# Kernel tuning notes

Hardware: AMD Instinct MI355X
Metric: run time of the kernel (lower is better)

The kernel has to match this reference:

```python
import jax, jax.numpy as jnp
import numpy as np
from collections import defaultdict

H = 24; W = 24          # patch grid
B0 = 64                 # original batch (len(batch_id))
B = 128                 # total batch incl. augmented copies
C_IN = 256; HID = 128; HEADS_S = 2; OUT = 256; K = 9; NCLS = 8


def _build_space_edges():
    # knn_graph on the normalized meshgrid coords; identical for every image -> offset copies.
    P = H * W
    coords = np.stack(np.meshgrid(np.arange(H), np.arange(W), indexing='ij'), -1).reshape(-1, 2).astype(np.float32)
    cn = coords / coords.max()
    d = ((cn[:, None, :] - cn[None, :, :]) ** 2).sum(-1)
    np.fill_diagonal(d, np.inf)              # loop=False
    nbr = np.argsort(d, axis=1)[:, :K]       # [P, K] neighbor (source) ids
    off = (np.arange(B0) * P)[:, None, None]
    src = (nbr[None] + off).reshape(-1)
    dst = (np.broadcast_to(np.arange(P)[:, None], (P, K))[None] + off).reshape(-1)
    return np.stack([src, dst]).astype(np.int64)


def _build_view_edges(bid_all):
    groups = defaultdict(list)
    for i, c in enumerate(bid_all.tolist()):
        groups[c].append(i)
    ei = []
    for c, mem in groups.items():
        for a in range(len(mem)):
            for b in range(a + 1, len(mem)):
                i, j = mem[a], mem[b]
                if i >= B0 and j >= B0:
                    continue               # skip augmented-augmented pairs
                ei.append((i, j)); ei.append((j, i))
    return np.array(ei, dtype=np.int64).T


def setup_inputs() -> dict:
    key = jax.random.key(0)
    ks = jax.random.split(key, 8)
    bid = np.repeat(np.arange(NCLS), B0 // NCLS).astype(np.int64)
    bid_all = np.concatenate([bid, bid])
    s = 0.05
    return {
        'x': jax.random.normal(ks[0], (B, C_IN, H, W), jnp.float32),
        'batch_id_all': jnp.asarray(bid_all),
        'batch_id': jnp.asarray(bid),
        'edge_index_space': jnp.asarray(_build_space_edges()),
        'edge_index_view': jnp.asarray(_build_view_edges(bid_all)),
        'W_space': jax.random.normal(ks[1], (C_IN, HEADS_S * HID), jnp.float32) * s,
        'att_src_space': jax.random.normal(ks[2], (HEADS_S, HID), jnp.float32) * s,
        'att_dst_space': jax.random.normal(ks[3], (HEADS_S, HID), jnp.float32) * s,
        'bias_space': jnp.zeros((HEADS_S * HID,), jnp.float32),
        'W_view': jax.random.normal(ks[4], (HEADS_S * HID, OUT), jnp.float32) * s,
        'att_src_view': jax.random.normal(ks[5], (1, OUT), jnp.float32) * s,
        'att_dst_view': jax.random.normal(ks[6], (1, OUT), jnp.float32) * s,
        'bias_view': jnp.zeros((OUT,), jnp.float32),
    }


def _gat(xn, edges, Wm, a_src, a_dst, bias, heads, outc):
    # PyG GATConv: linear -> per-edge leaky_relu attn -> segment softmax over dst -> scatter-add
    N = xn.shape[0]
    loops = jnp.arange(N, dtype=edges.dtype)              # add_self_loops=True
    src = jnp.concatenate([edges[0], loops])
    dst = jnp.concatenate([edges[1], loops])
    h = (xn @ Wm).reshape(N, heads, outc)                 # [N, H, C]
    a_s = jnp.sum(h * a_src[None], -1)                    # [N, H]
    a_d = jnp.sum(h * a_dst[None], -1)
    e = jax.nn.leaky_relu(a_s[src] + a_d[dst], 0.2)       # [E, H]
    m = jax.ops.segment_max(e, dst, num_segments=N)
    ee = jnp.exp(e - m[dst])
    ssum = jax.ops.segment_sum(ee, dst, num_segments=N)
    alpha = ee / (ssum[dst] + 1e-16)
    out = jax.ops.segment_sum(h[src] * alpha[..., None], dst, num_segments=N)
    return out.reshape(N, heads * outc) + bias            # concat=True


def reference(x, batch_id_all, batch_id, edge_index_space, edge_index_view,
              W_space, att_src_space, att_dst_space, bias_space,
              W_view, att_src_view, att_dst_view, bias_view):
    P = H * W
    node = x[:B0].transpose(0, 2, 3, 1).reshape(-1, C_IN)                # [B0*P, C_in]
    x_space = _gat(node, edge_index_space, W_space, att_src_space,
                   att_dst_space, bias_space, HEADS_S, HID)              # [B0*P, 256]
    emb = x_space.reshape(B0, P, -1).mean(axis=1)                        # per-image mean pool
    emb_all = emb[jnp.arange(B) % B0]                                    # augmented i -> i % B0
    feat = _gat(emb_all, edge_index_view, W_view, att_src_view,
                att_dst_view, bias_view, 1, OUT)                         # [B, 256]
    C = feat.shape[1]
    x_view = 0.5 * x_space.reshape(B0, P, C) + 0.5 * feat[:B0][:, None, :]
    # torch does .reshape(-1, C).view(B, C, H, W): a raw row-major reinterpret
    return x_view.reshape(B0, C, H, W)
```

## Files before the change

kernel.cpp:

```cpp
#include <hip/hip_runtime.h>

#define PGRID 576
#define NB0   64
#define CIN   256
#define KNN   9
#define NNODE (NB0 * PGRID)

typedef __attribute__((ext_vector_type(8))) short short8;
typedef __attribute__((ext_vector_type(4))) float f32x4;

__device__ __forceinline__ float bf2f(unsigned short u) {
    union { unsigned int i; float f; } v; v.i = ((unsigned int)u) << 16; return v.f;
}
__device__ __forceinline__ unsigned short f2b(float f) {
    unsigned int u = __float_as_uint(f);
    return (unsigned short)((u + 0x7FFFu + ((u >> 16) & 1u)) >> 16);
}

__global__ __launch_bounds__(256) void prep_w(const float* __restrict__ W,
                                              unsigned short* __restrict__ Wt) {
    __shared__ float tile[64][65];
    const int c0 = blockIdx.x * 64, j0 = blockIdx.y * 64;
    const int t = threadIdx.x, lo = t % 64, hi = t / 64;
#pragma unroll
    for (int r = 0; r < 16; ++r)
        tile[r * 4 + hi][lo] = W[(size_t)(c0 + r * 4 + hi) * 256 + j0 + lo];
    __syncthreads();
#pragma unroll
    for (int r = 0; r < 16; ++r)
        Wt[(size_t)(j0 + r * 4 + hi) * 256 + c0 + lo] = f2b(tile[lo][r * 4 + hi]);
}

__global__ __launch_bounds__(256) void gemm_fused(
    const float* __restrict__ x, const unsigned short* __restrict__ Wt,
    const float* __restrict__ att_src, const float* __restrict__ att_dst,
    unsigned short* __restrict__ h, float* __restrict__ as_, float* __restrict__ ad_) {
    __shared__ char ldsB[65536];
    const int bx = blockIdx.x;
    const int t  = threadIdx.x;
    const int b  = bx / 9;
    const int p0 = (bx % 9) * 64;
    const int n0 = bx * 64;
    const int l = t & 63, w = t >> 6;
    const int l4 = l >> 4, l15 = l & 15;
    const float* xb = x + (size_t)b * (CIN * PGRID);

    const int prow = p0 + w * 16 + l15;
    float a0[64];
#pragma unroll
    for (int ch = 0; ch < 2; ++ch)
#pragma unroll
        for (int q = 0; q < 4; ++q)
#pragma unroll
            for (int jj = 0; jj < 8; ++jj) {
                int c = ch * 128 + q * 32 + l4 * 8 + jj;
                a0[ch * 32 + q * 8 + jj] = xb[(size_t)c * PGRID + prow];
            }
    {
        const int jrow = t >> 4, g = t & 15;
#pragma unroll
        for (int i = 0; i < 16; ++i) {
            int j  = i * 16 + jrow;
            int gs = (g & 8) | ((g & 7) ^ (j & 7));
            __builtin_amdgcn_global_load_lds(
                (const char*)Wt + (size_t)j * 512 + gs * 16,
                ldsB + i * 4096 + (t & 192) * 16, 16, 0, 0);
        }
    }
    short8 apk[8];
#pragma unroll
    for (int cq = 0; cq < 8; ++cq) {
        short8 v;
#pragma unroll
        for (int jj = 0; jj < 8; ++jj) v[jj] = (short)f2b(a0[cq * 8 + jj]);
        apk[cq] = v;
    }
    f32x4 acc[16] = {};
    __syncthreads();
#pragma unroll
    for (int q = 0; q < 4; ++q) {
        const int gr = q * 4 + l4;
#pragma unroll
        for (int f = 0; f < 16; ++f) {
            int j  = f * 16 + l15;
            int gp = (gr & 8) | ((gr & 7) ^ (j & 7));
            short8 bf = *(const short8*)(ldsB + j * 256 + gp * 16);
            acc[f] = __builtin_amdgcn_mfma_f32_16x16x32_bf16(apk[q], bf, acc[f], 0, 0, 0);
        }
    }
    __syncthreads();
    {
        const int jrow = t >> 4, g = t & 15;
#pragma unroll
        for (int i = 0; i < 16; ++i) {
            int j  = i * 16 + jrow;
            int gs = (g & 8) | ((g & 7) ^ (j & 7));
            __builtin_amdgcn_global_load_lds(
                (const char*)Wt + (size_t)j * 512 + 256 + gs * 16,
                ldsB + i * 4096 + (t & 192) * 16, 16, 0, 0);
        }
    }
    __syncthreads();
#pragma unroll
    for (int q = 0; q < 4; ++q) {
        const int gr = q * 4 + l4;
#pragma unroll
        for (int f = 0; f < 16; ++f) {
            int j  = f * 16 + l15;
            int gp = (gr & 8) | ((gr & 7) ^ (j & 7));
            short8 bf = *(const short8*)(ldsB + j * 256 + gp * 16);
            acc[f] = __builtin_amdgcn_mfma_f32_16x16x32_bf16(apk[4 + q], bf, acc[f], 0, 0, 0);
        }
    }
    const int nb = n0 + w * 16 + l4 * 4;
#pragma unroll
    for (int f = 0; f < 16; ++f)
#pragma unroll
        for (int r = 0; r < 4; ++r)
            h[(size_t)(nb + r) * 256 + l15 + f * 16] = f2b(acc[f][r]);

    float av[16], dvv[16];
#pragma unroll
    for (int f = 0; f < 16; ++f) {
        av[f]  = att_src[f * 16 + l15];
        dvv[f] = att_dst[f * 16 + l15];
    }
#pragma unroll
    for (int r = 0; r < 4; ++r) {
        float s0 = 0.f, s1 = 0.f, d0 = 0.f, d1 = 0.f;
#pragma unroll
        for (int f = 0; f < 8; ++f)  { s0 += acc[f][r] * av[f];  d0 += acc[f][r] * dvv[f]; }
#pragma unroll
        for (int f = 8; f < 16; ++f) { s1 += acc[f][r] * av[f];  d1 += acc[f][r] * dvv[f]; }
#pragma unroll
        for (int m = 1; m < 16; m <<= 1) {
            s0 += __shfl_xor(s0, m); s1 += __shfl_xor(s1, m);
            d0 += __shfl_xor(d0, m); d1 += __shfl_xor(d1, m);
        }
        if (l15 == 0) {
            int n = nb + r;
            as_[n * 2] = s0; as_[n * 2 + 1] = s1;
            ad_[n * 2] = d0; ad_[n * 2 + 1] = d1;
        }
    }
}

__global__ __launch_bounds__(256) void space_gather(
    const unsigned short* __restrict__ h, const float* __restrict__ as_,
    const float* __restrict__ ad_, const int* __restrict__ esrc,
    const float* __restrict__ bias, unsigned short* __restrict__ xsb) {
    __shared__ int   s_src[2][10];
    __shared__ float s_e[2][10][2];
    const int t = threadIdx.x;
    const int node = t >> 7;
    const int idx  = t & 127;
    const int n = blockIdx.x * 2 + node;
    if (idx < 10) {
        int src = (idx < 9) ? esrc[(size_t)n * KNN + idx] : n;
        s_src[node][idx] = src;
        float e0 = as_[src * 2]     + ad_[n * 2];
        float e1 = as_[src * 2 + 1] + ad_[n * 2 + 1];
        s_e[node][idx][0] = e0 >= 0.f ? e0 : 0.2f * e0;
        s_e[node][idx][1] = e1 >= 0.f ? e1 : 0.2f * e1;
    }
    __syncthreads();
    const int j2 = idx * 2;
    const int head = idx >> 6;
    float m = -1e30f;
#pragma unroll
    for (int k = 0; k < 10; ++k) m = fmaxf(m, s_e[node][k][head]);
    float wgt[10]; float ssum = 0.f;
#pragma unroll
    for (int k = 0; k < 10; ++k) { wgt[k] = __expf(s_e[node][k][head] - m); ssum += wgt[k]; }
    const float inv = 1.f / (ssum + 1e-16f);
    float o0 = 0.f, o1 = 0.f;
#pragma unroll
    for (int k = 0; k < 10; ++k) {
        unsigned int v = *(const unsigned int*)(h + (size_t)s_src[node][k] * 256 + j2);
        o0 += wgt[k] * bf2f((unsigned short)(v & 0xffff));
        o1 += wgt[k] * bf2f((unsigned short)(v >> 16));
    }
    o0 = o0 * inv + bias[j2];
    o1 = o1 * inv + bias[j2 + 1];
    unsigned int pack = (unsigned int)f2b(o0) | ((unsigned int)f2b(o1) << 16);
    *(unsigned int*)(xsb + (size_t)n * 256 + j2) = pack;
}

__global__ __launch_bounds__(256) void pool_partial(const unsigned short* __restrict__ xsb,
                                                    float* __restrict__ embp) {
    __shared__ float red[2][256];
    const int b = blockIdx.x, seg = blockIdx.y;
    const int t = threadIdx.x;
    const int j2 = (t & 127) * 2, half = t >> 7;
    const unsigned short* base = xsb + ((size_t)b * PGRID + seg * 64 + half * 32) * 256 + j2;
    float s0 = 0.f, s1 = 0.f;
#pragma unroll 8
    for (int p = 0; p < 32; ++p) {
        unsigned int v = *(const unsigned int*)(base + (size_t)p * 256);
        s0 += bf2f((unsigned short)(v & 0xffff));
        s1 += bf2f((unsigned short)(v >> 16));
    }
    red[half][j2] = s0; red[half][j2 + 1] = s1;
    __syncthreads();
    if (half == 0) {
        float2 r;
        r.x = s0 + red[1][j2];
        r.y = s1 + red[1][j2 + 1];
        *(float2*)(embp + ((size_t)b * 9 + seg) * 256 + j2) = r;
    }
}

__global__ __launch_bounds__(256) void view_linear(const float* __restrict__ embp,
                                                   const float* __restrict__ Wv,
                                                   const float* __restrict__ att_s,
                                                   const float* __restrict__ att_d,
                                                   float* __restrict__ hv,
                                                   float* __restrict__ asv,
                                                   float* __restrict__ adv) {
    __shared__ float er[256];
    __shared__ float red[2][256];
    const int i = blockIdx.x;
    const int j = threadIdx.x;
    const int i64 = i & 63;
    float s = 0.f;
#pragma unroll
    for (int seg = 0; seg < 9; ++seg) s += embp[((size_t)i64 * 9 + seg) * 256 + j];
    er[j] = s * (1.f / 576.f);
    __syncthreads();
    float acc = 0.f;
    for (int c = 0; c < 256; ++c) acc += er[c] * Wv[c * 256 + j];
    hv[(size_t)i * 256 + j] = acc;
    red[0][j] = acc * att_s[j];
    red[1][j] = acc * att_d[j];
    __syncthreads();
    for (int off = 128; off > 0; off >>= 1) {
        if (j < off) { red[0][j] += red[0][j + off]; red[1][j] += red[1][j + off]; }
        __syncthreads();
    }
    if (j == 0) { asv[i] = red[0][0]; adv[i] = red[1][0]; }
}

__global__ __launch_bounds__(256) void view_gather(const float* __restrict__ hv,
                                                   const float* __restrict__ asv,
                                                   const float* __restrict__ adv,
                                                   const int* __restrict__ ev,
                                                   int Ev,
                                                   const float* __restrict__ bias,
                                                   float* __restrict__ feat) {
    __shared__ int cnt;
    __shared__ int s_src[32];
    const int d = blockIdx.x;
    const int t = threadIdx.x;
    if (t == 0) cnt = 0;
    __syncthreads();
    for (int e = t; e < Ev; e += 256) {
        if (ev[Ev + e] == d) {
            int pos = atomicAdd(&cnt, 1);
            s_src[pos] = ev[e];
        }
    }
    __syncthreads();
    const int ns = cnt;
    const float adval = adv[d];
    float m = -1e30f;
    float ev_[16];
#pragma unroll 1
    for (int k = 0; k < ns; ++k) {
        float e = asv[s_src[k]] + adval;
        e = e >= 0.f ? e : 0.2f * e;
        ev_[k] = e;
        m = fmaxf(m, e);
    }
    float eself = asv[d] + adval;
    eself = eself >= 0.f ? eself : 0.2f * eself;
    m = fmaxf(m, eself);
    float ssum = 0.f;
#pragma unroll 1
    for (int k = 0; k < ns; ++k) { ev_[k] = __expf(ev_[k] - m); ssum += ev_[k]; }
    float wself = __expf(eself - m);
    ssum += wself;
    const float inv = 1.f / (ssum + 1e-16f);
    float out = 0.f;
#pragma unroll 1
    for (int k = 0; k < ns; ++k) out += ev_[k] * hv[(size_t)s_src[k] * 256 + t];
    out += wself * hv[(size_t)d * 256 + t];
    feat[d * 256 + t] = out * inv + bias[t];
}

__global__ __launch_bounds__(256) void combine(const unsigned short* __restrict__ xsb,
                                               const float* __restrict__ feat,
                                               float* __restrict__ out, int ntot4) {
    int i = blockIdx.x * blockDim.x + threadIdx.x;
    if (i >= ntot4) return;
    size_t f = (size_t)i * 4;
    int b = (int)(f / (PGRID * 256));
    int j = (int)(f & 255);
    uint2 v = *(const uint2*)(xsb + f);
    float4 fb = *(const float4*)(feat + b * 256 + j);
    float4 o;
    o.x = 0.5f * (bf2f((unsigned short)(v.x & 0xffff)) + fb.x);
    o.y = 0.5f * (bf2f((unsigned short)(v.x >> 16))   + fb.y);
    o.z = 0.5f * (bf2f((unsigned short)(v.y & 0xffff)) + fb.z);
    o.w = 0.5f * (bf2f((unsigned short)(v.y >> 16))   + fb.w);
    *(float4*)(out + f) = o;
}

extern "C" void kernel_launch(void* const* d_in, const int* in_sizes, int n_in,
                              void* d_out, int out_size, void* d_ws, size_t ws_size,
                              hipStream_t stream) {
    const float* x        = (const float*)d_in[0];
    const int*   e_space  = (const int*)d_in[3];
    const int*   e_view   = (const int*)d_in[4];
    const float* W_space  = (const float*)d_in[5];
    const float* att_ss   = (const float*)d_in[6];
    const float* att_ds   = (const float*)d_in[7];
    const float* bias_s   = (const float*)d_in[8];
    const float* W_view   = (const float*)d_in[9];
    const float* att_sv   = (const float*)d_in[10];
    const float* att_dv   = (const float*)d_in[11];
    const float* bias_v   = (const float*)d_in[12];
    float* out = (float*)d_out;

    const int Ev = in_sizes[4] / 2;

    char* ws = (char*)d_ws;
    unsigned short* hbf = (unsigned short*)ws;
    unsigned short* Wt  = (unsigned short*)(ws + 18874368);
    unsigned short* xsb = (unsigned short*)(ws + 18874368 + 131072);
    float* as_  = (float*)(ws + 2 * 18874368 + 131072);
    float* ad_  = as_ + NNODE * 2;
    float* embp = ad_ + NNODE * 2;
    float* hv   = embp + 64 * 9 * 256;
    float* asv  = hv  + 128 * 256;
    float* adv  = asv + 128;
    float* feat = adv + 128;

    prep_w<<<dim3(4, 4), 256, 0, stream>>>(W_space, Wt);
    gemm_fused<<<576, 256, 0, stream>>>(x, Wt, att_ss, att_ds, hbf, as_, ad_);
    space_gather<<<NNODE / 2, 256, 0, stream>>>(hbf, as_, ad_, e_space, bias_s, xsb);
    pool_partial<<<dim3(NB0, 9), 256, 0, stream>>>(xsb, embp);
    view_linear<<<128, 256, 0, stream>>>(embp, W_view, att_sv, att_dv, hv, asv, adv);
    view_gather<<<NB0, 256, 0, stream>>>(hv, asv, adv, e_view, Ev, bias_v, feat);

    const int ntot4 = NB0 * PGRID * 256 / 4;
    combine<<<(ntot4 + 255) / 256, 256, 0, stream>>>(xsb, feat, out, ntot4);
}
```

Baseline: 209.9 us.

## Drop LDS staging in GEMM, widen gather and pool vector loads

The GEMM kernel no longer stages the bf16 weight in LDS. It swaps the MFMA operands so each lane loads weight fragments straight from global/L2 and writes h rows as packed 8-byte stores. The attention-score reduction now needs fewer shuffles. The space gather drops shared memory and syncthreads, handling one node per wavefront with 4 nodes per block and 8-byte loads, and pool_partial uses 4-element vector loads. This cuts LDS traffic, barriers and store transactions, but every block re-reads the weight from cache.

```diff
diff --git a/kernel.cpp b/kernel.cpp
--- a/kernel.cpp
+++ b/kernel.cpp
@@ -35,7 +35,6 @@
     const float* __restrict__ x, const unsigned short* __restrict__ Wt,
     const float* __restrict__ att_src, const float* __restrict__ att_dst,
     unsigned short* __restrict__ h, float* __restrict__ as_, float* __restrict__ ad_) {
-    __shared__ char ldsB[65536];
     const int bx = blockIdx.x;
     const int t  = threadIdx.x;
     const int b  = bx / 9;
@@ -44,29 +43,16 @@
     const int l = t & 63, w = t >> 6;
     const int l4 = l >> 4, l15 = l & 15;
     const float* xb = x + (size_t)b * (CIN * PGRID);
-
     const int prow = p0 + w * 16 + l15;
+
     float a0[64];
 #pragma unroll
-    for (int ch = 0; ch < 2; ++ch)
-#pragma unroll
-        for (int q = 0; q < 4; ++q)
-#pragma unroll
-            for (int jj = 0; jj < 8; ++jj) {
-                int c = ch * 128 + q * 32 + l4 * 8 + jj;
-                a0[ch * 32 + q * 8 + jj] = xb[(size_t)c * PGRID + prow];
-            }
-    {
-        const int jrow = t >> 4, g = t & 15;
-#pragma unroll
-        for (int i = 0; i < 16; ++i) {
-            int j  = i * 16 + jrow;
-            int gs = (g & 8) | ((g & 7) ^ (j & 7));
-            __builtin_amdgcn_global_load_lds(
-                (const char*)Wt + (size_t)j * 512 + gs * 16,
-                ldsB + i * 4096 + (t & 192) * 16, 16, 0, 0);
+    for (int cq = 0; cq < 8; ++cq)
+#pragma unroll
+        for (int jj = 0; jj < 8; ++jj) {
+            int c = cq * 32 + l4 * 8 + jj;
+            a0[cq * 8 + jj] = xb[(size_t)c * PGRID + prow];
         }
-    }
     short8 apk[8];
 #pragma unroll
     for (int cq = 0; cq < 8; ++cq) {
@@ -75,73 +61,46 @@
         for (int jj = 0; jj < 8; ++jj) v[jj] = (short)f2b(a0[cq * 8 + jj]);
         apk[cq] = v;
     }
+
     f32x4 acc[16] = {};
-    __syncthreads();
-#pragma unroll
-    for (int q = 0; q < 4; ++q) {
-        const int gr = q * 4 + l4;
+    const unsigned short* wbase = Wt + (size_t)l15 * 256 + l4 * 8;
+#pragma unroll
+    for (int q = 0; q < 8; ++q) {
 #pragma unroll
         for (int f = 0; f < 16; ++f) {
-            int j  = f * 16 + l15;
-            int gp = (gr & 8) | ((gr & 7) ^ (j & 7));
-            short8 bf = *(const short8*)(ldsB + j * 256 + gp * 16);
-            acc[f] = __builtin_amdgcn_mfma_f32_16x16x32_bf16(apk[q], bf, acc[f], 0, 0, 0);
+            short8 wf = *(const short8*)(wbase + (size_t)f * 4096 + q * 32);
+            acc[f] = __builtin_amdgcn_mfma_f32_16x16x32_bf16(wf, apk[q], acc[f], 0, 0, 0);
         }
     }
-    __syncthreads();
-    {
-        const int jrow = t >> 4, g = t & 15;
-#pragma unroll
-        for (int i = 0; i < 16; ++i) {
-            int j  = i * 16 + jrow;
-            int gs = (g & 8) | ((g & 7) ^ (j & 7));
-            __builtin_amdgcn_global_load_lds(
-                (const char*)Wt + (size_t)j * 512 + 256 + gs * 16,
-                ldsB + i * 4096 + (t & 192) * 16, 16, 0, 0);
-        }
-    }
-    __syncthreads();
-#pragma unroll
-    for (int q = 0; q < 4; ++q) {
-        const int gr = q * 4 + l4;
-#pragma unroll
-        for (int f = 0; f < 16; ++f) {
-            int j  = f * 16 + l15;
-            int gp = (gr & 8) | ((gr & 7) ^ (j & 7));
-            short8 bf = *(const short8*)(ldsB + j * 256 + gp * 16);
-            acc[f] = __builtin_amdgcn_mfma_f32_16x16x32_bf16(apk[4 + q], bf, acc[f], 0, 0, 0);
-        }
-    }
-    const int nb = n0 + w * 16 + l4 * 4;
-#pragma unroll
-    for (int f = 0; f < 16; ++f)
-#pragma unroll
-        for (int r = 0; r < 4; ++r)
-            h[(size_t)(nb + r) * 256 + l15 + f * 16] = f2b(acc[f][r]);
-
-    float av[16], dvv[16];
+
+    unsigned short* hrow = h + (size_t)(n0 + w * 16 + l15) * 256 + l4 * 4;
 #pragma unroll
     for (int f = 0; f < 16; ++f) {
-        av[f]  = att_src[f * 16 + l15];
-        dvv[f] = att_dst[f * 16 + l15];
-    }
-#pragma unroll
-    for (int r = 0; r < 4; ++r) {
-        float s0 = 0.f, s1 = 0.f, d0 = 0.f, d1 = 0.f;
-#pragma unroll
-        for (int f = 0; f < 8; ++f)  { s0 += acc[f][r] * av[f];  d0 += acc[f][r] * dvv[f]; }
-#pragma unroll
-        for (int f = 8; f < 16; ++f) { s1 += acc[f][r] * av[f];  d1 += acc[f][r] * dvv[f]; }
-#pragma unroll
-        for (int m = 1; m < 16; m <<= 1) {
-            s0 += __shfl_xor(s0, m); s1 += __shfl_xor(s1, m);
-            d0 += __shfl_xor(d0, m); d1 += __shfl_xor(d1, m);
-        }
-        if (l15 == 0) {
-            int n = nb + r;
-            as_[n * 2] = s0; as_[n * 2 + 1] = s1;
-            ad_[n * 2] = d0; ad_[n * 2 + 1] = d1;
-        }
+        uint2 pk;
+        pk.x = (unsigned int)f2b(acc[f][0]) | ((unsigned int)f2b(acc[f][1]) << 16);
+        pk.y = (unsigned int)f2b(acc[f][2]) | ((unsigned int)f2b(acc[f][3]) << 16);
+        *(uint2*)(hrow + f * 16) = pk;
+    }
+
+    float s0 = 0.f, s1 = 0.f, d0 = 0.f, d1 = 0.f;
+#pragma unroll
+    for (int f = 0; f < 16; ++f) {
+        float4 av = *(const float4*)(att_src + f * 16 + l4 * 4);
+        float4 dv = *(const float4*)(att_dst + f * 16 + l4 * 4);
+        float ss = acc[f][0] * av.x + acc[f][1] * av.y + acc[f][2] * av.z + acc[f][3] * av.w;
+        float dd = acc[f][0] * dv.x + acc[f][1] * dv.y + acc[f][2] * dv.z + acc[f][3] * dv.w;
+        if (f < 8) { s0 += ss; d0 += dd; } else { s1 += ss; d1 += dd; }
+    }
+    s0 += __shfl_xor(s0, 16); s0 += __shfl_xor(s0, 32);
+    s1 += __shfl_xor(s1, 16); s1 += __shfl_xor(s1, 32);
+    d0 += __shfl_xor(d0, 16); d0 += __shfl_xor(d0, 32);
+    d1 += __shfl_xor(d1, 16); d1 += __shfl_xor(d1, 32);
+    if (l < 16) {
+        int n = n0 + w * 16 + l;
+        float2 sv; sv.x = s0; sv.y = s1;
+        float2 dv2; dv2.x = d0; dv2.y = d1;
+        *(float2*)(as_ + 2 * n) = sv;
+        *(float2*)(ad_ + 2 * n) = dv2;
     }
 }
 
@@ -149,64 +108,76 @@
     const unsigned short* __restrict__ h, const float* __restrict__ as_,
     const float* __restrict__ ad_, const int* __restrict__ esrc,
     const float* __restrict__ bias, unsigned short* __restrict__ xsb) {
-    __shared__ int   s_src[2][10];
-    __shared__ float s_e[2][10][2];
     const int t = threadIdx.x;
-    const int node = t >> 7;
-    const int idx  = t & 127;
-    const int n = blockIdx.x * 2 + node;
-    if (idx < 10) {
-        int src = (idx < 9) ? esrc[(size_t)n * KNN + idx] : n;
-        s_src[node][idx] = src;
-        float e0 = as_[src * 2]     + ad_[n * 2];
-        float e1 = as_[src * 2 + 1] + ad_[n * 2 + 1];
-        s_e[node][idx][0] = e0 >= 0.f ? e0 : 0.2f * e0;
-        s_e[node][idx][1] = e1 >= 0.f ? e1 : 0.2f * e1;
-    }
-    __syncthreads();
-    const int j2 = idx * 2;
-    const int head = idx >> 6;
+    const int g = t >> 6, l = t & 63;
+    const int n = blockIdx.x * 4 + g;
+    int srcs[10];
+#pragma unroll
+    for (int k = 0; k < 9; ++k) srcs[k] = esrc[n * 9 + k];
+    srcs[9] = n;
+    const int head = l >> 5;
+    const float adv = ad_[n * 2 + head];
+    float e[10];
     float m = -1e30f;
 #pragma unroll
-    for (int k = 0; k < 10; ++k) m = fmaxf(m, s_e[node][k][head]);
-    float wgt[10]; float ssum = 0.f;
-#pragma unroll
-    for (int k = 0; k < 10; ++k) { wgt[k] = __expf(s_e[node][k][head] - m); ssum += wgt[k]; }
+    for (int k = 0; k < 10; ++k) {
+        float ev = as_[srcs[k] * 2 + head] + adv;
+        ev = ev >= 0.f ? ev : 0.2f * ev;
+        e[k] = ev; m = fmaxf(m, ev);
+    }
+    float ssum = 0.f;
+#pragma unroll
+    for (int k = 0; k < 10; ++k) { e[k] = __expf(e[k] - m); ssum += e[k]; }
     const float inv = 1.f / (ssum + 1e-16f);
-    float o0 = 0.f, o1 = 0.f;
+    const int j4 = l * 4;
+    float o0 = 0.f, o1 = 0.f, o2 = 0.f, o3 = 0.f;
 #pragma unroll
     for (int k = 0; k < 10; ++k) {
-        unsigned int v = *(const unsigned int*)(h + (size_t)s_src[node][k] * 256 + j2);
-        o0 += wgt[k] * bf2f((unsigned short)(v & 0xffff));
-        o1 += wgt[k] * bf2f((unsigned short)(v >> 16));
-    }
-    o0 = o0 * inv + bias[j2];
-    o1 = o1 * inv + bias[j2 + 1];
-    unsigned int pack = (unsigned int)f2b(o0) | ((unsigned int)f2b(o1) << 16);
-    *(unsigned int*)(xsb + (size_t)n * 256 + j2) = pack;
+        uint2 v = *(const uint2*)(h + (size_t)srcs[k] * 256 + j4);
+        o0 += e[k] * bf2f((unsigned short)(v.x & 0xffff));
+        o1 += e[k] * bf2f((unsigned short)(v.x >> 16));
+        o2 += e[k] * bf2f((unsigned short)(v.y & 0xffff));
+        o3 += e[k] * bf2f((unsigned short)(v.y >> 16));
+    }
+    float4 bi = *(const float4*)(bias + j4);
+    o0 = o0 * inv + bi.x; o1 = o1 * inv + bi.y;
+    o2 = o2 * inv + bi.z; o3 = o3 * inv + bi.w;
+    uint2 pk;
+    pk.x = (unsigned int)f2b(o0) | ((unsigned int)f2b(o1) << 16);
+    pk.y = (unsigned int)f2b(o2) | ((unsigned int)f2b(o3) << 16);
+    *(uint2*)(xsb + (size_t)n * 256 + j4) = pk;
 }
 
 __global__ __launch_bounds__(256) void pool_partial(const unsigned short* __restrict__ xsb,
                                                     float* __restrict__ embp) {
-    __shared__ float red[2][256];
+    __shared__ float red[4][256];
     const int b = blockIdx.x, seg = blockIdx.y;
     const int t = threadIdx.x;
-    const int j2 = (t & 127) * 2, half = t >> 7;
-    const unsigned short* base = xsb + ((size_t)b * PGRID + seg * 64 + half * 32) * 256 + j2;
-    float s0 = 0.f, s1 = 0.f;
-#pragma unroll 8
-    for (int p = 0; p < 32; ++p) {
-        unsigned int v = *(const unsigned int*)(base + (size_t)p * 256);
-        s0 += bf2f((unsigned short)(v & 0xffff));
-        s1 += bf2f((unsigned short)(v >> 16));
-    }
-    red[half][j2] = s0; red[half][j2 + 1] = s1;
-    __syncthreads();
-    if (half == 0) {
-        float2 r;
-        r.x = s0 + red[1][j2];
-        r.y = s1 + red[1][j2 + 1];
-        *(float2*)(embp + ((size_t)b * 9 + seg) * 256 + j2) = r;
+    const int l = t & 63, sub = t >> 6;
+    const int j4 = l * 4;
+    const unsigned short* base = xsb + ((size_t)b * PGRID + seg * 64 + sub * 16) * 256 + j4;
+    float s0 = 0.f, s1 = 0.f, s2 = 0.f, s3 = 0.f;
+#pragma unroll
+    for (int p = 0; p < 16; ++p) {
+        uint2 v = *(const uint2*)(base + (size_t)p * 256);
+        s0 += bf2f((unsigned short)(v.x & 0xffff));
+        s1 += bf2f((unsigned short)(v.x >> 16));
+        s2 += bf2f((unsigned short)(v.y & 0xffff));
+        s3 += bf2f((unsigned short)(v.y >> 16));
+    }
+    float4 sv; sv.x = s0; sv.y = s1; sv.z = s2; sv.w = s3;
+    *(float4*)(&red[sub][j4]) = sv;
+    __syncthreads();
+    if (sub == 0) {
+        float4 a = *(float4*)(&red[1][j4]);
+        float4 c = *(float4*)(&red[2][j4]);
+        float4 d = *(float4*)(&red[3][j4]);
+        float4 r;
+        r.x = s0 + a.x + c.x + d.x;
+        r.y = s1 + a.y + c.y + d.y;
+        r.z = s2 + a.z + c.z + d.z;
+        r.w = s3 + a.w + c.w + d.w;
+        *(float4*)(embp + ((size_t)b * 9 + seg) * 256 + j4) = r;
     }
 }
 
@@ -337,7 +308,7 @@
 
     prep_w<<<dim3(4, 4), 256, 0, stream>>>(W_space, Wt);
     gemm_fused<<<576, 256, 0, stream>>>(x, Wt, att_ss, att_ds, hbf, as_, ad_);
-    space_gather<<<NNODE / 2, 256, 0, stream>>>(hbf, as_, ad_, e_space, bias_s, xsb);
+    space_gather<<<NNODE / 4, 256, 0, stream>>>(hbf, as_, ad_, e_space, bias_s, xsb);
     pool_partial<<<dim3(NB0, 9), 256, 0, stream>>>(xsb, embp);
     view_linear<<<128, 256, 0, stream>>>(embp, W_view, att_sv, att_dv, hv, asv, adv);
     view_gather<<<NB0, 256, 0, stream>>>(hv, asv, adv, e_view, Ev, bias_v, feat);
```

Result: slower. 239.8 us (+14.3%).
